# Optimization experiments

Measured on AMD Instinct MI355X. Metric: run time of the kernel, lower is better.

Reference implementation:

```python
import jax, jax.numpy as jnp
import numpy as np

N_APP = 100000
N_ATTR = 50000
E = 500000
D_IN = 128
D_H = 128
D_OUT = 2


def _sage(h_src, h_dst, src, dst, ew, W_self, W_neigh, b, n_dst):
    # DGL SAGEConv('mean') with edge_weight: m_e = ew_e * h_src[src_e];
    # h_neigh_v = sum_e->v m_e / in_degree(v); out = h_dst@W_self + h_neigh@W_neigh + b
    # (feat_drop=0.2 is identity in eval mode)
    m = h_src[src] * ew[:, None]                                   # [E, d]
    s = jax.ops.segment_sum(m, dst, num_segments=n_dst)            # [n_dst, d]
    deg = jax.ops.segment_sum(jnp.ones_like(ew), dst, num_segments=n_dst)
    h_neigh = s / jnp.maximum(deg, 1.0)[:, None]
    return h_dst @ W_self + h_neigh @ W_neigh + b


def _forward(x_app, x_attr, ew0, ew1, ew2,
             Wself1, Wneigh1, b1, Wself2, Wneigh2, b2, Wc, bc,
             src0, dst0, src1, dst1, src2, dst2):
    # ---- layer 1 (HeteroGraphConv, aggregate='sum' over relations per dst ntype) ----
    h_attr = _sage(x_app, x_attr, src0, dst0, ew0, Wself1[0], Wneigh1[0], b1[0], N_ATTR)
    h_app = (_sage(x_attr, x_app, src1, dst1, ew1, Wself1[1], Wneigh1[1], b1[1], N_APP)
             + _sage(x_app, x_app, src2, dst2, ew2, Wself1[2], Wneigh1[2], b1[2], N_APP))
    h_attr = jax.nn.relu(h_attr)
    h_app = jax.nn.relu(h_app)
    # ---- layer 2 ----
    h_attr2 = _sage(h_app, h_attr, src0, dst0, ew0, Wself2[0], Wneigh2[0], b2[0], N_ATTR)
    h_app2 = (_sage(h_attr, h_app, src1, dst1, ew1, Wself2[1], Wneigh2[1], b2[1], N_APP)
              + _sage(h_app, h_app, src2, dst2, ew2, Wself2[2], Wneigh2[2], b2[2], N_APP))
    del h_attr2  # second layer output on 'attribute' is unused by classify
    # ---- classify on 'application' ----
    return h_app2 @ Wc + bc


def setup_inputs() -> dict:
    key = jax.random.key(0)
    ks = jax.random.split(key, 20)
    sc = 1.0 / np.sqrt(D_H)
    return {
        "x_app": jax.random.normal(ks[0], (N_APP, D_IN), jnp.float32),
        "x_attr": jax.random.normal(ks[1], (N_ATTR, D_IN), jnp.float32),
        "ew0": jax.random.uniform(ks[2], (E,), jnp.float32),
        "ew1": jax.random.uniform(ks[3], (E,), jnp.float32),
        "ew2": jax.random.uniform(ks[4], (E,), jnp.float32),
        "Wself1": jax.random.normal(ks[5], (3, D_IN, D_H), jnp.float32) * sc,
        "Wneigh1": jax.random.normal(ks[6], (3, D_IN, D_H), jnp.float32) * sc,
        "b1": jax.random.normal(ks[7], (3, D_H), jnp.float32) * 0.01,
        "Wself2": jax.random.normal(ks[8], (3, D_H, D_H), jnp.float32) * sc,
        "Wneigh2": jax.random.normal(ks[9], (3, D_H, D_H), jnp.float32) * sc,
        "b2": jax.random.normal(ks[10], (3, D_H), jnp.float32) * 0.01,
        "Wc": jax.random.normal(ks[11], (D_H, D_OUT), jnp.float32) * sc,
        "bc": jax.random.normal(ks[12], (D_OUT,), jnp.float32) * 0.01,
        "src0": jax.random.randint(ks[13], (E,), 0, N_APP, jnp.int32),
        "dst0": jax.random.randint(ks[14], (E,), 0, N_ATTR, jnp.int32),
        "src1": jax.random.randint(ks[15], (E,), 0, N_ATTR, jnp.int32),
        "dst1": jax.random.randint(ks[16], (E,), 0, N_APP, jnp.int32),
        "src2": jax.random.randint(ks[17], (E,), 0, N_APP, jnp.int32),
        "dst2": jax.random.randint(ks[18], (E,), 0, N_APP, jnp.int32),
    }


def reference(x_app, x_attr, ew0, ew1, ew2,
              Wself1, Wneigh1, b1, Wself2, Wneigh2, b2, Wc, bc,
              src0, dst0, src1, dst1, src2, dst2):
    return _forward(x_app, x_attr, ew0, ew1, ew2,
                    Wself1, Wneigh1, b1, Wself2, Wneigh2, b2, Wc, bc,
                    src0, dst0, src1, dst1, src2, dst2)
```

## Files before the change

kernel.cpp:

```cpp
#include <hip/hip_runtime.h>

#define NAPP  100000
#define NATTR 50000
#define NE    500000
#define D     128
#define NTOT  (NATTR + 2 * NAPP)
#define SCHUNK 1024
#define SNB   ((NTOT + SCHUNK - 1) / SCHUNK)
#define EG8   ((NE / 8 + 255) / 256)
#define GB_APP  ((NAPP + 63) / 64)
#define GB_ATTR ((NATTR + 63) / 64)
#define ECAP  1024
#define ZERO_B 64

typedef __attribute__((ext_vector_type(8))) short bfrag;
typedef __attribute__((ext_vector_type(4))) float f32x4;

__device__ __forceinline__ short bf16_rn(float x) {
    union { float f; unsigned u; } a; a.f = x;
    unsigned r = (a.u + 0x7fffu + ((a.u >> 16) & 1u)) >> 16;
    return (short)r;
}
__device__ __forceinline__ float bf16_to_f(short s) {
    union { float f; unsigned u; } a;
    a.u = ((unsigned)(unsigned short)s) << 16;
    return a.f;
}

__device__ __forceinline__ void split2(float x, float y, unsigned& hw, unsigned& lw) {
    union { float f; unsigned u; } ax, ay;
    ax.f = x; ay.f = y;
    unsigned hx = (ax.u + 0x7fffu + ((ax.u >> 16) & 1u)) >> 16;
    unsigned hy = (ay.u + 0x7fffu + ((ay.u >> 16) & 1u)) >> 16;
    union { unsigned u; float f; } fx, fy;
    fx.u = hx << 16; fy.u = hy << 16;
    union { float f; unsigned u; } rx, ry;
    rx.f = x - fx.f; ry.f = y - fy.f;
    unsigned lx = (rx.u + 0x7fffu + ((rx.u >> 16) & 1u)) >> 16;
    unsigned ly = (ry.u + 0x7fffu + ((ry.u >> 16) & 1u)) >> 16;
    hw = (hy << 16) | (hx & 0xffffu);
    lw = (ly << 16) | (lx & 0xffffu);
}

__global__ __launch_bounds__(256) void hist3_kernel(
        const int* __restrict__ d0, const int* __restrict__ d1, const int* __restrict__ d2,
        int* __restrict__ h0, int* __restrict__ h1, int* __restrict__ h2,
        short* __restrict__ r0, short* __restrict__ r1, short* __restrict__ r2) {
    int b = blockIdx.x;
    int rel = b / EG8;
    int i8 = (b - rel * EG8) * 256 + threadIdx.x;
    if (i8 >= NE / 8) return;
    const int* dst = (rel == 0) ? d0 : (rel == 1) ? d1 : d2;
    int* h = (rel == 0) ? h0 : (rel == 1) ? h1 : h2;
    short* rk = (rel == 0) ? r0 : (rel == 1) ? r1 : r2;
    int4 da = *((const int4*)dst + 2 * i8);
    int4 db = *((const int4*)dst + 2 * i8 + 1);
    union { short s[8]; int4 v; } u;
    u.s[0] = (short)atomicAdd(&h[da.x], 1);
    u.s[1] = (short)atomicAdd(&h[da.y], 1);
    u.s[2] = (short)atomicAdd(&h[da.z], 1);
    u.s[3] = (short)atomicAdd(&h[da.w], 1);
    u.s[4] = (short)atomicAdd(&h[db.x], 1);
    u.s[5] = (short)atomicAdd(&h[db.y], 1);
    u.s[6] = (short)atomicAdd(&h[db.z], 1);
    u.s[7] = (short)atomicAdd(&h[db.w], 1);
    *((int4*)rk + i8) = u.v;
}

__global__ __launch_bounds__(256) void scan_partial_kernel(const int* __restrict__ cur,
                                                           int* __restrict__ bsum) {
    int b = blockIdx.x, t = threadIdx.x;
    int4 v = *((const int4*)(cur + b * SCHUNK) + t);
    int s = v.x + v.y + v.z + v.w;
    __shared__ int sd[256];
    sd[t] = s;
    __syncthreads();
    for (int off = 128; off > 0; off >>= 1) {
        if (t < off) sd[t] += sd[t + off];
        __syncthreads();
    }
    if (t == 0) bsum[b] = sd[0];
}

__global__ __launch_bounds__(256) void scan_final_kernel(const int* __restrict__ cur,
        const int* __restrict__ bsum, int* __restrict__ rp0, int* __restrict__ rp1,
        int* __restrict__ rp2) {
    int b = blockIdx.x, t = threadIdx.x;
    __shared__ int sb[256];
    int vb = (t < SNB) ? bsum[t] : 0;
    sb[t] = vb;
    __syncthreads();
    for (int off = 1; off < 256; off <<= 1) {
        int u = (t >= off) ? sb[t - off] : 0;
        __syncthreads();
        sb[t] += u;
        __syncthreads();
    }
    const int boffb = sb[b] - bsum[b];
    __syncthreads();
    int base = b * SCHUNK + t * 4;
    int4 v = *(const int4*)(cur + base);
    int s = v.x + v.y + v.z + v.w;
    __shared__ int sd[256];
    sd[t] = s;
    __syncthreads();
    for (int off = 1; off < 256; off <<= 1) {
        int u = (t >= off) ? sd[t - off] : 0;
        __syncthreads();
        sd[t] += u;
        __syncthreads();
    }
    int pre = boffb + sd[t] - s;
    int ex[4];
    ex[0] = pre;
    ex[1] = ex[0] + v.x;
    ex[2] = ex[1] + v.y;
    ex[3] = ex[2] + v.z;
    #pragma unroll
    for (int i = 0; i < 4; i++) {
        int idx = base + i;
        if (idx < NTOT) {
            int* rp; int loc; int rbase;
            if (idx < NATTR)             { rp = rp0; loc = idx;                 rbase = 0; }
            else if (idx < NATTR + NAPP) { rp = rp1; loc = idx - NATTR;        rbase = NE; }
            else                         { rp = rp2; loc = idx - NATTR - NAPP; rbase = 2 * NE; }
            rp[loc] = ex[i] - rbase;
        }
    }
    if (b == 0 && t == 0) { rp0[NATTR] = NE; rp1[NAPP] = NE; rp2[NAPP] = NE; }
}

__global__ __launch_bounds__(256) void scatter3_kernel(
        const int* __restrict__ s0, const int* __restrict__ d0, const float* __restrict__ e0,
        const short* __restrict__ r0, const int* __restrict__ rp0, int2* __restrict__ cw0,
        const int* __restrict__ s1, const int* __restrict__ d1, const float* __restrict__ e1,
        const short* __restrict__ r1, const int* __restrict__ rp1, int2* __restrict__ cw1,
        const int* __restrict__ s2, const int* __restrict__ d2, const float* __restrict__ e2,
        const short* __restrict__ r2, const int* __restrict__ rp2, int2* __restrict__ cw2) {
    int b = blockIdx.x;
    int rel = b / EG8;
    int i8 = (b - rel * EG8) * 256 + threadIdx.x;
    if (i8 >= NE / 8) return;
    const int* src; const int* dst; const float* ew; const short* rk; const int* rp; int2* cw;
    if (rel == 0)      { src = s0; dst = d0; ew = e0; rk = r0; rp = rp0; cw = cw0; }
    else if (rel == 1) { src = s1; dst = d1; ew = e1; rk = r1; rp = rp1; cw = cw1; }
    else               { src = s2; dst = d2; ew = e2; rk = r2; rp = rp2; cw = cw2; }
    int4 sa = *((const int4*)src + 2 * i8);
    int4 sb = *((const int4*)src + 2 * i8 + 1);
    int4 da = *((const int4*)dst + 2 * i8);
    int4 db = *((const int4*)dst + 2 * i8 + 1);
    float4 ea = *((const float4*)ew + 2 * i8);
    float4 eb = *((const float4*)ew + 2 * i8 + 1);
    union { short s[8]; int4 v; } u;
    u.v = *((const int4*)rk + i8);
    cw[rp[da.x] + u.s[0]] = make_int2(sa.x, __float_as_int(ea.x));
    cw[rp[da.y] + u.s[1]] = make_int2(sa.y, __float_as_int(ea.y));
    cw[rp[da.z] + u.s[2]] = make_int2(sa.z, __float_as_int(ea.z));
    cw[rp[da.w] + u.s[3]] = make_int2(sa.w, __float_as_int(ea.w));
    cw[rp[db.x] + u.s[4]] = make_int2(sb.x, __float_as_int(eb.x));
    cw[rp[db.y] + u.s[5]] = make_int2(sb.y, __float_as_int(eb.y));
    cw[rp[db.z] + u.s[6]] = make_int2(sb.z, __float_as_int(eb.z));
    cw[rp[db.w] + u.s[7]] = make_int2(sb.w, __float_as_int(eb.w));
}

__global__ __launch_bounds__(256) void pack_kernel(
        const float* __restrict__ Wself1, const float* __restrict__ Wneigh1,
        const float* __restrict__ Wself2, const float* __restrict__ Wneigh2,
        const float* __restrict__ b1, const float* __restrict__ b2,
        const float* __restrict__ Wc, const float* __restrict__ bc,
        short* __restrict__ PBh, short* __restrict__ PBl,
        float* __restrict__ b1s, float* __restrict__ b2s,
        float* __restrict__ Cs, float* __restrict__ C1, float* __restrict__ C2,
        float* __restrict__ bconst, int* __restrict__ cur) {
    int m = blockIdx.x;
    if (m >= 9) {
        int idx = (m - 9) * 256 + threadIdx.x;
        const int n4 = (SNB * SCHUNK) / 4;
        for (int i = idx; i < n4; i += ZERO_B * 256)
            *((int4*)cur + i) = make_int4(0, 0, 0, 0);
        return;
    }
    if (m == 8) {
        int tid = threadIdx.x;
        int k = tid >> 1, j = tid & 1;
        const float* Wn1 = Wneigh2 + D * D;
        const float* Wn2 = Wneigh2 + 2 * D * D;
        const float* Ws1 = Wself2 + D * D;
        const float* Ws2 = Wself2 + 2 * D * D;
        float ss = 0.f, s1 = 0.f, s2 = 0.f;
        for (int tt = 0; tt < D; tt++) {
            float wc = Wc[tt * 2 + j];
            ss += (Ws1[k * D + tt] + Ws2[k * D + tt]) * wc;
            s1 += Wn1[k * D + tt] * wc;
            s2 += Wn2[k * D + tt] * wc;
        }
        Cs[tid] = ss; C1[tid] = s1; C2[tid] = s2;
        if (tid < 2) {
            float s = bc[tid];
            for (int tt = 0; tt < D; tt++)
                s += (b2[D + tt] + b2[2 * D + tt]) * Wc[tt * 2 + tid];
            bconst[tid] = s;
        }
        return;
    }
    const float* srcA; const float* srcB = nullptr;
    switch (m) {
        case 0: srcA = Wself1; break;
        case 1: srcA = Wneigh1; break;
        case 2: srcA = Wself1 + D * D; srcB = Wself1 + 2 * D * D; break;
        case 3: srcA = Wneigh1 + D * D; break;
        case 4: srcA = Wneigh1 + 2 * D * D; break;
        case 5: srcA = Wself2 + D * D; srcB = Wself2 + 2 * D * D; break;
        case 6: srcA = Wneigh2 + D * D; break;
        default: srcA = Wneigh2 + 2 * D * D; break;
    }
    short* oh = PBh + (size_t)m * D * D;
    short* ol = PBl + (size_t)m * D * D;
    for (int i = threadIdx.x; i < D * D; i += 256) {
        int k = i >> 7, n = i & 127;
        float v = srcA[i];
        if (srcB) v += srcB[i];
        short hi = bf16_rn(v);
        short lo = bf16_rn(v - bf16_to_f(hi));
        int kc = k >> 5, q = (k >> 3) & 3, j = k & 7, nt = n >> 4, c = n & 15;
        int pos = (((kc * 8 + nt) * 64) + q * 16 + c) * 8 + j;
        oh[pos] = hi;
        ol[pos] = lo;
    }
    if (m == 0 && threadIdx.x < D) {
        int t = threadIdx.x;
        b1s[t] = b1[D + t] + b1[2 * D + t];
        b2s[t] = b2[D + t] + b2[2 * D + t];
    }
}

#define ASTR 128
template<int NG>
__device__ __forceinline__ void fused_body(
        const float* __restrict__ in0, const short* __restrict__ B0h, const short* __restrict__ B0l,
        const float* __restrict__ x1, const int* __restrict__ rp1, const int2* __restrict__ cw1,
        const short* __restrict__ B1h, const short* __restrict__ B1l,
        const float* __restrict__ x2, const int* __restrict__ rp2, const int2* __restrict__ cw2,
        const short* __restrict__ B2h, const short* __restrict__ B2l,
        const float* __restrict__ bias,
        const float* __restrict__ Ccol0, const float* __restrict__ Ccol1,
        float* __restrict__ zo0, float* __restrict__ zo1,
        int nrows, int row0, float* At, int2* eds) {
    const int t = threadIdx.x;
    const int w = t >> 6, lane = t & 63;
    const int q = lane >> 4, c = lane & 15;
    const int myrow = row0 + w * 16 + c;
    const int arow = min(myrow, nrows - 1);

    f32x4 acc[8];
    #pragma unroll
    for (int nt = 0; nt < 8; nt++) acc[nt] = (f32x4){0.f, 0.f, 0.f, 0.f};

    {
        const float* __restrict__ arp = in0 + (size_t)arow * D;
        const bfrag* __restrict__ Bh = (const bfrag*)B0h;
        const bfrag* __restrict__ Bl = (const bfrag*)B0l;
        #pragma unroll
        for (int kc = 0; kc < 4; kc++) {
            float4 a0 = *(const float4*)(arp + kc * 32 + q * 8);
            float4 a1 = *(const float4*)(arp + kc * 32 + q * 8 + 4);
            union { unsigned u[4]; bfrag v; } ahu, alu;
            split2(a0.x, a0.y, ahu.u[0], alu.u[0]);
            split2(a0.z, a0.w, ahu.u[1], alu.u[1]);
            split2(a1.x, a1.y, ahu.u[2], alu.u[2]);
            split2(a1.z, a1.w, ahu.u[3], alu.u[3]);
            bfrag ah = ahu.v, al = alu.v;
            const bfrag* bh = Bh + kc * 512 + lane;
            const bfrag* bl = Bl + kc * 512 + lane;
            #pragma unroll
            for (int nt = 0; nt < 8; nt++) {
                bfrag vh = bh[nt * 64];
                bfrag vl = bl[nt * 64];
                acc[nt] = __builtin_amdgcn_mfma_f32_16x16x32_bf16(ah, vh, acc[nt], 0, 0, 0);
                acc[nt] = __builtin_amdgcn_mfma_f32_16x16x32_bf16(ah, vl, acc[nt], 0, 0, 0);
                acc[nt] = __builtin_amdgcn_mfma_f32_16x16x32_bf16(al, vh, acc[nt], 0, 0, 0);
            }
        }
    }

    const int grp = t >> 5, l32 = t & 31;
    #pragma unroll
    for (int g = 0; g < NG; g++) {
        const float* __restrict__ xs = (g == 0) ? x1 : x2;
        const int* __restrict__ rp   = (g == 0) ? rp1 : rp2;
        const int2* __restrict__ cw  = (g == 0) ? cw1 : cw2;
        const short* __restrict__ Bhp = (g == 0) ? B1h : B2h;
        const short* __restrict__ Blp = (g == 0) ? B1l : B2l;

        if (g > 0) __syncthreads();
        const int eb0 = rp[row0];
        const int eb1 = rp[min(row0 + 64, nrows)];
        const int ecnt = eb1 - eb0;
        const bool staged = (ecnt < ECAP);
        if (staged) {
            for (int i = t; i < ecnt; i += 256) eds[i] = cw[eb0 + i];
            if (t == 0) eds[ecnt] = make_int2(0, 0);
        }
        __syncthreads();

        {
            const int r0g = row0 + grp * 8;
            int bnd[9];
            #pragma unroll
            for (int i = 0; i < 9; i++) bnd[i] = rp[min(r0g + i, nrows)];
            #pragma unroll
            for (int p = 0; p < 4; p++) {
                const int A0 = bnd[2 * p],     A1 = bnd[2 * p + 1];
                const int B0 = bnd[2 * p + 1], B1 = bnd[2 * p + 2];
                float4 aA = make_float4(0.f, 0.f, 0.f, 0.f);
                float4 aB = make_float4(0.f, 0.f, 0.f, 0.f);
                const int lastA = min(max(A1 - 1, A0), NE - 1);
                const int lastB = min(max(B1 - 1, B0), NE - 1);
                int jA = A0, jB = B0;
                while (jA < A1 || jB < B1) {
                    int2 ed[8];
                    if (staged) {
                        #pragma unroll
                        for (int u = 0; u < 4; u++)
                            ed[u] = eds[min(min(jA + u, lastA) - eb0, ecnt)];
                        #pragma unroll
                        for (int u = 0; u < 4; u++)
                            ed[4 + u] = eds[min(min(jB + u, lastB) - eb0, ecnt)];
                    } else {
                        #pragma unroll
                        for (int u = 0; u < 4; u++) ed[u] = cw[min(jA + u, lastA)];
                        #pragma unroll
                        for (int u = 0; u < 4; u++) ed[4 + u] = cw[min(jB + u, lastB)];
                    }
                    float wt[8];
                    #pragma unroll
                    for (int u = 0; u < 4; u++)
                        wt[u] = (jA + u < A1) ? __int_as_float(ed[u].y) : 0.f;
                    #pragma unroll
                    for (int u = 0; u < 4; u++)
                        wt[4 + u] = (jB + u < B1) ? __int_as_float(ed[4 + u].y) : 0.f;
                    float4 v[8];
                    #pragma unroll
                    for (int u = 0; u < 8; u++)
                        v[u] = *(const float4*)(xs + (size_t)ed[u].x * D + l32 * 4);
                    aA.x += wt[0] * v[0].x + wt[1] * v[1].x + wt[2] * v[2].x + wt[3] * v[3].x;
                    aA.y += wt[0] * v[0].y + wt[1] * v[1].y + wt[2] * v[2].y + wt[3] * v[3].y;
                    aA.z += wt[0] * v[0].z + wt[1] * v[1].z + wt[2] * v[2].z + wt[3] * v[3].z;
                    aA.w += wt[0] * v[0].w + wt[1] * v[1].w + wt[2] * v[2].w + wt[3] * v[3].w;
                    aB.x += wt[4] * v[4].x + wt[5] * v[5].x + wt[6] * v[6].x + wt[7] * v[7].x;
                    aB.y += wt[4] * v[4].y + wt[5] * v[5].y + wt[6] * v[6].y + wt[7] * v[7].y;
                    aB.z += wt[4] * v[4].z + wt[5] * v[5].z + wt[6] * v[6].z + wt[7] * v[7].z;
                    aB.w += wt[4] * v[4].w + wt[5] * v[5].w + wt[6] * v[6].w + wt[7] * v[7].w;
                    jA += 4; jB += 4;
                }
                const float invA = 1.0f / (float)max(A1 - A0, 1);
                const float invB = 1.0f / (float)max(B1 - B0, 1);
                aA.x *= invA; aA.y *= invA; aA.z *= invA; aA.w *= invA;
                aB.x *= invB; aB.y *= invB; aB.z *= invB; aB.w *= invB;
                const int lrA = grp * 8 + 2 * p;
                const int lrB = lrA + 1;
                *(float4*)&At[lrA * ASTR + ((l32 ^ ((lrA & 3) << 1)) << 2)] = aA;
                *(float4*)&At[lrB * ASTR + ((l32 ^ ((lrB & 3) << 1)) << 2)] = aB;
            }
        }
        __syncthreads();

        const bfrag* __restrict__ Bh = (const bfrag*)Bhp;
        const bfrag* __restrict__ Bl = (const bfrag*)Blp;
        const int rloc = w * 16 + c;
        const int sw = (rloc & 3) << 1;
        const float* __restrict__ arow_lds = &At[rloc * ASTR];
        #pragma unroll
        for (int kc = 0; kc < 4; kc++) {
            const int g0 = kc * 8 + q * 2;
            float4 a0 = *(const float4*)(arow_lds + ((g0 ^ sw) << 2));
            float4 a1 = *(const float4*)(arow_lds + (((g0 + 1) ^ sw) << 2));
            union { unsigned u[4]; bfrag v; } ahu, alu;
            split2(a0.x, a0.y, ahu.u[0], alu.u[0]);
            split2(a0.z, a0.w, ahu.u[1], alu.u[1]);
            split2(a1.x, a1.y, ahu.u[2], alu.u[2]);
            split2(a1.z, a1.w, ahu.u[3], alu.u[3]);
            bfrag ah = ahu.v, al = alu.v;
            const bfrag* bh = Bh + kc * 512 + lane;
            const bfrag* bl = Bl + kc * 512 + lane;
            #pragma unroll
            for (int nt = 0; nt < 8; nt++) {
                bfrag vh = bh[nt * 64];
                bfrag vl = bl[nt * 64];
                acc[nt] = __builtin_amdgcn_mfma_f32_16x16x32_bf16(ah, vh, acc[nt], 0, 0, 0);
                acc[nt] = __builtin_amdgcn_mfma_f32_16x16x32_bf16(ah, vl, acc[nt], 0, 0, 0);
                acc[nt] = __builtin_amdgcn_mfma_f32_16x16x32_bf16(al, vh, acc[nt], 0, 0, 0);
            }
        }
    }

    float c00[8], c01[8], c10[8], c11[8], bvv[8];
    #pragma unroll
    for (int nt = 0; nt < 8; nt++) {
        float2 v0 = *(const float2*)(Ccol0 + (nt * 16 + c) * 2);
        c00[nt] = v0.x; c01[nt] = v0.y;
        if (NG == 2) {
            float2 v1 = *(const float2*)(Ccol1 + (nt * 16 + c) * 2);
            c10[nt] = v1.x; c11[nt] = v1.y;
        }
        bvv[nt] = bias[nt * 16 + c];
    }
    #pragma unroll
    for (int r = 0; r < 4; r++) {
        int row = row0 + w * 16 + q * 4 + r;
        float s0 = 0.f, s1 = 0.f, t0 = 0.f, t1 = 0.f;
        #pragma unroll
        for (int nt = 0; nt < 8; nt++) {
            float h = fmaxf(acc[nt][r] + bvv[nt], 0.f);
            s0 += h * c00[nt]; s1 += h * c01[nt];
            if (NG == 2) { t0 += h * c10[nt]; t1 += h * c11[nt]; }
        }
        #pragma unroll
        for (int off = 1; off < 16; off <<= 1) {
            s0 += __shfl_xor(s0, off);
            s1 += __shfl_xor(s1, off);
            if (NG == 2) { t0 += __shfl_xor(t0, off); t1 += __shfl_xor(t1, off); }
        }
        if (c == 0 && row < nrows) {
            *(float2*)(zo0 + (size_t)row * 2) = make_float2(s0, s1);
            if (NG == 2) *(float2*)(zo1 + (size_t)row * 2) = make_float2(t0, t1);
        }
    }
}

__global__ __launch_bounds__(256, 4) void fused_all_kernel(
        const float* __restrict__ xapp, const float* __restrict__ xattr,
        const short* __restrict__ PBh, const short* __restrict__ PBl,
        const int* __restrict__ rp0, const int2* __restrict__ cw0,
        const int* __restrict__ rp1, const int2* __restrict__ cw1,
        const int* __restrict__ rp2, const int2* __restrict__ cw2,
        const float* __restrict__ b1, const float* __restrict__ b1s,
        const float* __restrict__ Cs, const float* __restrict__ C2,
        const float* __restrict__ C1,
        float* __restrict__ zs, float* __restrict__ z2, float* __restrict__ za) {
    __shared__ __align__(16) float At[64 * ASTR];
    __shared__ __align__(16) int2 eds[ECAP];
    const size_t MM = (size_t)D * D;
    int b = blockIdx.x;
    if (b < GB_APP) {
        fused_body<2>(xapp, PBh + 2 * MM, PBl + 2 * MM,
                      xattr, rp1, cw1, PBh + 3 * MM, PBl + 3 * MM,
                      xapp,  rp2, cw2, PBh + 4 * MM, PBl + 4 * MM,
                      b1s, Cs, C2, zs, z2, NAPP, b * 64, At, eds);
    } else {
        int bb = b - GB_APP;
        fused_body<1>(xattr, PBh, PBl,
                      xapp, rp0, cw0, PBh + 1 * MM, PBl + 1 * MM,
                      nullptr, nullptr, nullptr, nullptr, nullptr,
                      b1, C1, nullptr, za, nullptr, NATTR, bb * 64, At, eds);
    }
}

__global__ __launch_bounds__(256) void final_out_kernel(
        const float* __restrict__ zs, const float* __restrict__ za,
        const float* __restrict__ z2,
        const int* __restrict__ rp1, const int2* __restrict__ cw1,
        const int* __restrict__ rp2, const int2* __restrict__ cw2,
        const float* __restrict__ bconst, float* __restrict__ out, int n) {
    int r = (blockIdx.x * 256 + threadIdx.x) >> 2;
    int l = threadIdx.x & 3;
    if (r >= n) return;
    int s0 = rp1[r], s1 = rp1[r + 1];
    float q0 = 0.f, q1 = 0.f;
    for (int j = s0 + l; j < s1; j += 4) {
        int2 e = cw1[j];
        float w = __int_as_float(e.y);
        float2 v = *(const float2*)(za + (size_t)e.x * 2);
        q0 += w * v.x; q1 += w * v.y;
    }
    float inv1 = 1.0f / (float)max(s1 - s0, 1);
    float p0 = q0 * inv1, p1 = q1 * inv1;
    s0 = rp2[r]; s1 = rp2[r + 1];
    q0 = 0.f; q1 = 0.f;
    for (int j = s0 + l; j < s1; j += 4) {
        int2 e = cw2[j];
        float w = __int_as_float(e.y);
        float2 v = *(const float2*)(z2 + (size_t)e.x * 2);
        q0 += w * v.x; q1 += w * v.y;
    }
    float inv2 = 1.0f / (float)max(s1 - s0, 1);
    p0 += q0 * inv2; p1 += q1 * inv2;
    #pragma unroll
    for (int off = 1; off < 4; off <<= 1) {
        p0 += __shfl_xor(p0, off);
        p1 += __shfl_xor(p1, off);
    }
    if (l == 0) {
        float2 s = *(const float2*)(zs + (size_t)r * 2);
        out[(size_t)r * 2 + 0] = p0 + s.x + bconst[0];
        out[(size_t)r * 2 + 1] = p1 + s.y + bconst[1];
    }
}

extern "C" void kernel_launch(void* const* d_in, const int* in_sizes, int n_in,
                              void* d_out, int out_size, void* d_ws, size_t ws_size,
                              hipStream_t stream) {
    const float* x_app   = (const float*)d_in[0];
    const float* x_attr  = (const float*)d_in[1];
    const float* ew0     = (const float*)d_in[2];
    const float* ew1     = (const float*)d_in[3];
    const float* ew2     = (const float*)d_in[4];
    const float* Wself1  = (const float*)d_in[5];
    const float* Wneigh1 = (const float*)d_in[6];
    const float* b1      = (const float*)d_in[7];
    const float* Wself2  = (const float*)d_in[8];
    const float* Wneigh2 = (const float*)d_in[9];
    const float* b2      = (const float*)d_in[10];
    const float* Wc      = (const float*)d_in[11];
    const float* bc      = (const float*)d_in[12];
    const int* src0 = (const int*)d_in[13];
    const int* dst0 = (const int*)d_in[14];
    const int* src1 = (const int*)d_in[15];
    const int* dst1 = (const int*)d_in[16];
    const int* src2 = (const int*)d_in[17];
    const int* dst2 = (const int*)d_in[18];
    float* out = (float*)d_out;

    float* ws = (float*)d_ws;
    float* h_attr = ws;
    float* h_app  = h_attr + (size_t)NATTR * D;
    float* b1s    = h_app  + (size_t)NAPP * D;
    float* b2s    = b1s + D;
    float* za     = b2s + D;
    float* zsv    = za + (size_t)NATTR * 2;
    float* z2v    = zsv + (size_t)NAPP * 2;
    float* Cs     = z2v + (size_t)NAPP * 2;
    float* C1     = Cs + 256;
    float* C2     = C1 + 256;
    float* bconst = C2 + 256;
    int* cur  = (int*)(bconst + 4);
    int* cur0 = cur;
    int* cur1 = cur0 + NATTR;
    int* cur2 = cur1 + NAPP;
    int* rp0  = cur + SNB * SCHUNK;
    int* rp1  = rp0 + NATTR + 4;
    int* rp2  = rp1 + NAPP + 4;
    int* bsum = rp2 + NAPP + 4;
    int* boff = bsum + 256;
    int2* cw0 = (int2*)(boff + 256);
    int2* cw1 = cw0 + NE;
    int2* cw2 = cw1 + NE;
    short* PBh = (short*)(cw2 + NE);
    short* PBl = PBh + (size_t)8 * D * D;
    short* rank0 = (short*)h_attr;
    short* rank1 = rank0 + NE;
    short* rank2 = rank1 + NE;

    pack_kernel<<<9 + ZERO_B, 256, 0, stream>>>(Wself1, Wneigh1, Wself2, Wneigh2,
                                                b1, b2, Wc, bc, PBh, PBl, b1s, b2s,
                                                Cs, C1, C2, bconst, cur);

    hist3_kernel<<<3 * EG8, 256, 0, stream>>>(dst0, dst1, dst2, cur0, cur1, cur2,
                                              rank0, rank1, rank2);
    scan_partial_kernel<<<SNB, 256, 0, stream>>>(cur, bsum);
    scan_final_kernel<<<SNB, 256, 0, stream>>>(cur, bsum, rp0, rp1, rp2);
    scatter3_kernel<<<3 * EG8, 256, 0, stream>>>(
        src0, dst0, ew0, rank0, rp0, cw0,
        src1, dst1, ew1, rank1, rp1, cw1,
        src2, dst2, ew2, rank2, rp2, cw2);

    fused_all_kernel<<<GB_APP + GB_ATTR, 256, 0, stream>>>(
        x_app, x_attr, PBh, PBl,
        rp0, cw0, rp1, cw1, rp2, cw2,
        b1, b1s, Cs, C2, C1, zsv, z2v, za);

    final_out_kernel<<<((size_t)NAPP * 4 + 255) / 256, 256, 0, stream>>>(
        zsv, za, z2v, rp1, cw1, rp2, cw2, bconst, out, NAPP);
}
```

Before: 413.9 us.

## Merge two-pass scan into one kernel and interleave final gather loops

Replaces the partial/final scan kernel pair with a single kernel in which each block recomputes all chunk sums (first threads each sum one 1024-element chunk) before its local scan. This removes one launch and the bsum round trip, at the cost of every block re-reading the whole count array. The final output kernel now walks both relations' edge lists in a single interleaved loop with clamped indices, so more independent gathers are in flight per iteration. ECAP is also lowered from 1024 to 896.

```diff
diff --git a/kernel.cpp b/kernel.cpp
--- a/kernel.cpp
+++ b/kernel.cpp
@@ -10,7 +10,7 @@
 #define EG8   ((NE / 8 + 255) / 256)
 #define GB_APP  ((NAPP + 63) / 64)
 #define GB_ATTR ((NATTR + 63) / 64)
-#define ECAP  1024
+#define ECAP  896
 #define ZERO_B 64
 
 typedef __attribute__((ext_vector_type(8))) short bfrag;
@@ -67,42 +67,35 @@
     *((int4*)rk + i8) = u.v;
 }
 
-__global__ __launch_bounds__(256) void scan_partial_kernel(const int* __restrict__ cur,
-                                                           int* __restrict__ bsum) {
-    int b = blockIdx.x, t = threadIdx.x;
-    int4 v = *((const int4*)(cur + b * SCHUNK) + t);
-    int s = v.x + v.y + v.z + v.w;
-    __shared__ int sd[256];
-    sd[t] = s;
-    __syncthreads();
-    for (int off = 128; off > 0; off >>= 1) {
-        if (t < off) sd[t] += sd[t + off];
-        __syncthreads();
-    }
-    if (t == 0) bsum[b] = sd[0];
-}
-
-__global__ __launch_bounds__(256) void scan_final_kernel(const int* __restrict__ cur,
-        const int* __restrict__ bsum, int* __restrict__ rp0, int* __restrict__ rp1,
-        int* __restrict__ rp2) {
+__global__ __launch_bounds__(256) void scan_all_kernel(const int* __restrict__ cur,
+        int* __restrict__ rp0, int* __restrict__ rp1, int* __restrict__ rp2) {
     int b = blockIdx.x, t = threadIdx.x;
     __shared__ int sb[256];
-    int vb = (t < SNB) ? bsum[t] : 0;
-    sb[t] = vb;
+    int s = 0;
+    if (t < SNB) {
+        const int4* p = (const int4*)(cur + t * SCHUNK);
+        #pragma unroll 4
+        for (int i = 0; i < SCHUNK / 4; i++) {
+            int4 v = p[i];
+            s += v.x + v.y + v.z + v.w;
+        }
+    }
+    sb[t] = (t < SNB) ? s : 0;
     __syncthreads();
+    const int ownsum = sb[b];
     for (int off = 1; off < 256; off <<= 1) {
         int u = (t >= off) ? sb[t - off] : 0;
         __syncthreads();
         sb[t] += u;
         __syncthreads();
     }
-    const int boffb = sb[b] - bsum[b];
+    const int boffb = sb[b] - ownsum;
     __syncthreads();
     int base = b * SCHUNK + t * 4;
     int4 v = *(const int4*)(cur + base);
-    int s = v.x + v.y + v.z + v.w;
+    int cs = v.x + v.y + v.z + v.w;
     __shared__ int sd[256];
-    sd[t] = s;
+    sd[t] = cs;
     __syncthreads();
     for (int off = 1; off < 256; off <<= 1) {
         int u = (t >= off) ? sd[t - off] : 0;
@@ -110,7 +103,7 @@
         sd[t] += u;
         __syncthreads();
     }
-    int pre = boffb + sd[t] - s;
+    int pre = boffb + sd[t] - cs;
     int ex[4];
     ex[0] = pre;
     ex[1] = ex[0] + v.x;
@@ -465,26 +458,28 @@
     int r = (blockIdx.x * 256 + threadIdx.x) >> 2;
     int l = threadIdx.x & 3;
     if (r >= n) return;
-    int s0 = rp1[r], s1 = rp1[r + 1];
-    float q0 = 0.f, q1 = 0.f;
-    for (int j = s0 + l; j < s1; j += 4) {
-        int2 e = cw1[j];
-        float w = __int_as_float(e.y);
-        float2 v = *(const float2*)(za + (size_t)e.x * 2);
-        q0 += w * v.x; q1 += w * v.y;
-    }
-    float inv1 = 1.0f / (float)max(s1 - s0, 1);
-    float p0 = q0 * inv1, p1 = q1 * inv1;
-    s0 = rp2[r]; s1 = rp2[r + 1];
-    q0 = 0.f; q1 = 0.f;
-    for (int j = s0 + l; j < s1; j += 4) {
-        int2 e = cw2[j];
-        float w = __int_as_float(e.y);
-        float2 v = *(const float2*)(z2 + (size_t)e.x * 2);
-        q0 += w * v.x; q1 += w * v.y;
-    }
-    float inv2 = 1.0f / (float)max(s1 - s0, 1);
-    p0 += q0 * inv2; p1 += q1 * inv2;
+    const int sA0 = rp1[r], sA1 = rp1[r + 1];
+    const int sB0 = rp2[r], sB1 = rp2[r + 1];
+    const int lastA = min(max(sA1 - 1, sA0), NE - 1);
+    const int lastB = min(max(sB1 - 1, sB0), NE - 1);
+    float a0 = 0.f, a1 = 0.f, b0 = 0.f, b1 = 0.f;
+    int jA = sA0 + l, jB = sB0 + l;
+    while (jA < sA1 || jB < sB1) {
+        int2 eA = cw1[min(jA, lastA)];
+        int2 eB = cw2[min(jB, lastB)];
+        float wA = (jA < sA1) ? __int_as_float(eA.y) : 0.f;
+        float wB = (jB < sB1) ? __int_as_float(eB.y) : 0.f;
+        float2 vA = *(const float2*)(za + (size_t)eA.x * 2);
+        float2 vB = *(const float2*)(z2 + (size_t)eB.x * 2);
+        a0 += wA * vA.x; a1 += wA * vA.y;
+        b0 += wB * vB.x; b1 += wB * vB.y;
+        jA += 4; jB += 4;
+    }
+    const float inv1 = 1.0f / (float)max(sA1 - sA0, 1);
+    const float inv2 = 1.0f / (float)max(sB1 - sB0, 1);
+    float p0 = a0 * inv1, p1 = a1 * inv1;
+    p0 += b0 * inv2;
+    p1 += b1 * inv2;
     #pragma unroll
     for (int off = 1; off < 4; off <<= 1) {
         p0 += __shfl_xor(p0, off);
@@ -557,8 +552,7 @@
 
     hist3_kernel<<<3 * EG8, 256, 0, stream>>>(dst0, dst1, dst2, cur0, cur1, cur2,
                                               rank0, rank1, rank2);
-    scan_partial_kernel<<<SNB, 256, 0, stream>>>(cur, bsum);
-    scan_final_kernel<<<SNB, 256, 0, stream>>>(cur, bsum, rp0, rp1, rp2);
+    scan_all_kernel<<<SNB, 256, 0, stream>>>(cur, rp0, rp1, rp2);
     scatter3_kernel<<<3 * EG8, 256, 0, stream>>>(
         src0, dst0, ew0, rank0, rp0, cw0,
         src1, dst1, ew1, rank1, rp1, cw1,
```

New measurement: 442.4 us. 6.9% more time.
